# Optimization experiments

Measured on AMD Instinct MI355X. Metric: run time of the kernel, lower is better.

Reference implementation:

```python
import jax, jax.numpy as jnp
import numpy as np

N, D, H, B, TOPK, M, NLAB = 200000, 512, 512, 256, 2, 100, 2000

def setup_inputs():
    rng = np.random.default_rng(0)
    features = rng.standard_normal((N, D)).astype(np.float32) * 0.05
    labels = rng.integers(0, NLAB, size=N).astype(np.int32)
    # fixed-shape cluster membership table (replaces dynamic features[labels==lab]
    # + randperm subsampling to max_cluster_num=100 in the torch loop)
    order = np.argsort(labels, kind='stable').astype(np.int32)
    counts = np.bincount(labels, minlength=NLAB)
    offs = np.concatenate([[0], np.cumsum(counts)]).astype(np.int64)
    cluster_members = np.zeros((NLAB, M), np.int32)
    cluster_mask = np.zeros((NLAB, M), np.bool_)
    for c in range(NLAB):
        k = int(min(counts[c], M))
        cluster_members[c, :k] = order[offs[c]:offs[c] + k]
        cluster_mask[c, :k] = True
    indexes = rng.integers(0, N, size=B).astype(np.int32)
    # neighbors guaranteed != indexes so neighbor labels are never the -1 placeholder
    neighbors = ((indexes[:, None] + 1 + rng.integers(0, N - 1, size=(B, TOPK))) % N).astype(np.int32)
    all_pred = rng.random((B, TOPK)).astype(np.float32)
    # GraphConv weight [2D,H] (cat(self, agg)), classifier Linear-PReLU-Linear(2)
    W1 = (rng.standard_normal((2 * D, H)) / np.sqrt(2 * D)).astype(np.float32)
    b1 = np.zeros(H, np.float32)
    W2 = (rng.standard_normal((H, H)) / np.sqrt(H)).astype(np.float32)
    b2 = np.zeros(H, np.float32)
    prelu_a = np.full(H, 0.25, np.float32)  # PReLU default init
    W3 = (rng.standard_normal((H, 2)) / np.sqrt(H)).astype(np.float32)
    b3 = np.zeros(2, np.float32)
    arrs = dict(features=features, labels=labels, indexes=indexes, neighbors=neighbors,
                all_pred=all_pred, cluster_members=cluster_members, cluster_mask=cluster_mask,
                W1=W1, b1=b1, W2=W2, b2=b2, prelu_a=prelu_a, W3=W3, b3=b3)
    return {k: jnp.asarray(v) for k, v in arrs.items()}

def _gcnl_loss(features, labels, indexes, neighbors, all_pred, cluster_members, cluster_mask,
               W1, b1, W2, b2, prelu_a, W3, b3):
    Bn = indexes.shape[0]
    sel = all_pred >= all_pred[:, :1]                    # neighbor kept if pred[:topk] >= pred[0]
    cand = labels[neighbors]                             # [B,2] candidate labels
    dup = (cand[:, 1] == cand[:, 0]) & sel[:, 0]         # torch.unique over the <=2 selected labels
    valid = jnp.stack([sel[:, 0], sel[:, 1] & ~dup], axis=1)  # [B,2]
    members = cluster_members[cand]                      # [B,2,M]
    # labels[indexes[i]] = -1 in the loop => sample never in its own cluster
    mmask = cluster_mask[cand] & (members != indexes[:, None, None])
    mfeats = features[members] * mmask[..., None].astype(features.dtype)  # [B,2,M,D] zero-padded
    x0 = features[indexes]                               # [B,D]
    x0k = jnp.broadcast_to(x0[:, None, None, :], (Bn, TOPK, 1, x0.shape[-1]))
    x = jnp.concatenate([x0k, mfeats], axis=2)           # [B,2,M+1,D] = cat(self, cluster)
    # adj = x @ x.T ; only row 0 feeds the loss (pred[0]), zero-padded rows contribute 0
    a0 = jnp.einsum('bkd,bkmd->bkm', x[:, :, 0], x)      # [B,2,M+1] adjacency row 0
    agg0 = jnp.einsum('bkm,bkmd->bkd', a0, x)            # MeanAggregator (A @ x) row 0
    cat0 = jnp.concatenate([x[:, :, 0], agg0], axis=-1)  # [B,2,2D]
    h0 = jax.nn.relu(jnp.einsum('bkd,df->bkf', cat0, W1) + b1)  # GraphConv row 0
    z = jnp.einsum('bkf,fg->bkg', h0, W2) + b2
    z = jnp.where(z >= 0, z, prelu_a * z)                # PReLU
    logits = jnp.einsum('bkg,gc->bkc', z, W3) + b3       # [B,2,2]
    gt = (cand == -1).astype(jnp.int32)                  # labels[idx] was -1 during the loop
    logp = jax.nn.log_softmax(logits, axis=-1)
    ce = -jnp.take_along_axis(logp, gt[..., None], axis=-1)[..., 0]  # [B,2]
    loss = jnp.sum(ce * valid.astype(ce.dtype)) / Bn
    return loss * 10.0

def reference(features, labels, indexes, neighbors, all_pred, cluster_members, cluster_mask,
              W1, b1, W2, b2, prelu_a, W3, b3):
    return _gcnl_loss(features, labels, indexes, neighbors, all_pred, cluster_members, cluster_mask,
                      W1, b1, W2, b2, prelu_a, W3, b3)
```

## Files before the change

### kernel.cpp

```cpp
#include <hip/hip_runtime.h>
#include <math.h>

#define N_PTS 200000
#define D 512
#define H 512
#define BATCH 256
#define TOPK 2
#define MCAP 100

typedef __attribute__((ext_vector_type(8))) short bf16x8;
typedef __attribute__((ext_vector_type(4))) float f32x4;

__device__ inline unsigned short f2bf(float f) {
    unsigned int u = __float_as_uint(f);
    u += 0x7FFFu + ((u >> 16) & 1u);
    return (unsigned short)(u >> 16);
}

__global__ __launch_bounds__(512, 4) void gather_prep_kernel(
    const float* __restrict__ features, const int* __restrict__ labels,
    const int* __restrict__ indexes, const int* __restrict__ neighbors,
    const float* __restrict__ all_pred, const int* __restrict__ cluster_members,
    const float* __restrict__ W1, const float* __restrict__ W2,
    unsigned short* __restrict__ W1t, unsigned short* __restrict__ W2t,
    unsigned short* __restrict__ cat0, float* __restrict__ validf, int* __restrict__ gts,
    float* __restrict__ out)
{
    int bid = blockIdx.x;
    int tid = threadIdx.x;

    if (bid >= 512) {
        __shared__ float tt[2][32][33];
        int t = (bid - 512) * 2 + (tid >> 8);
        int t256 = tid & 255;
        int tx = t256 & 31, ty = t256 >> 5;
        const float* src; unsigned short* dst; int R, C, bi;
        if (t < 512) { src = W1; dst = W1t; R = 1024; C = 512; bi = t; }
        else         { src = W2; dst = W2t; R = 512;  C = 512; bi = t - 512; }
        int nbc = C >> 5;
        int br = (bi / nbc) * 32, bc = (bi % nbc) * 32;
        int half = tid >> 8;
        #pragma unroll
        for (int i = 0; i < 32; i += 8)
            tt[half][ty + i][tx] = src[(size_t)(br + ty + i) * C + bc + tx];
        __syncthreads();
        #pragma unroll
        for (int i = 0; i < 32; i += 8)
            dst[(size_t)(bc + ty + i) * R + br + tx] = f2bf(tt[half][tx][ty + i]);
        return;
    }

    int bk = bid;
    int b = bk >> 1, k = bk & 1;
    int lane = tid & 63, w = tid >> 6;

    if (bk == 0 && tid == 0) out[0] = 0.0f;

    int idx  = indexes[b];
    int nb   = neighbors[b * TOPK + k];
    int c    = labels[nb];
    int lab0 = labels[0];

    const float4* frow0 = (const float4*)(features + (size_t)idx * D);
    float4 x0a = frow0[lane * 2];
    float4 x0b = frow0[lane * 2 + 1];

    const int NITER = 13;
    int   rowv[NITER];
    float wv[NITER];
    #pragma unroll
    for (int i = 0; i < NITER; ++i) {
        int m = w + i * 8;
        int row = idx; float wt = 0.0f;
        if (m == 0) {
            wt = 1.0f;
        } else if (m <= MCAP) {
            int mm = m - 1;
            int r2 = cluster_members[c * MCAP + mm];
            bool pad  = (r2 == 0) && !(c == lab0 && mm == 0);
            bool self = (r2 == idx);
            if (!pad && !self) { row = r2; wt = 1.0f; }
        }
        rowv[i] = row; wv[i] = wt;
    }

    float agg[8] = {0,0,0,0,0,0,0,0};

    const float4* fr0 = (const float4*)(features + (size_t)rowv[0] * D);
    float4 fa = fr0[lane * 2];
    float4 fb = fr0[lane * 2 + 1];
    #pragma unroll
    for (int i = 0; i < NITER; ++i) {
        float4 ca = fa, cb = fb;
        if (i + 1 < NITER) {
            const float4* nx = (const float4*)(features + (size_t)rowv[i + 1] * D);
            fa = nx[lane * 2];
            fb = nx[lane * 2 + 1];
        }
        float p = ca.x*x0a.x + ca.y*x0a.y + ca.z*x0a.z + ca.w*x0a.w
                + cb.x*x0b.x + cb.y*x0b.y + cb.z*x0b.z + cb.w*x0b.w;
        #pragma unroll
        for (int off = 32; off >= 1; off >>= 1) p += __shfl_xor(p, off);
        p *= wv[i];
        agg[0] += p * ca.x; agg[1] += p * ca.y; agg[2] += p * ca.z; agg[3] += p * ca.w;
        agg[4] += p * cb.x; agg[5] += p * cb.y; agg[6] += p * cb.z; agg[7] += p * cb.w;
    }

    __shared__ float aggl[8][D];
    #pragma unroll
    for (int j = 0; j < 8; ++j) aggl[w][lane * 8 + j] = agg[j];
    __syncthreads();

    unsigned short* crow = cat0 + (size_t)bk * (2 * D);
    if (w == 0) {
        union { unsigned short u[8]; uint4 q; } pk;
        pk.u[0] = f2bf(x0a.x); pk.u[1] = f2bf(x0a.y); pk.u[2] = f2bf(x0a.z); pk.u[3] = f2bf(x0a.w);
        pk.u[4] = f2bf(x0b.x); pk.u[5] = f2bf(x0b.y); pk.u[6] = f2bf(x0b.z); pk.u[7] = f2bf(x0b.w);
        ((uint4*)crow)[lane] = pk.q;
    }
    {
        float v = aggl[0][tid] + aggl[1][tid] + aggl[2][tid] + aggl[3][tid]
                + aggl[4][tid] + aggl[5][tid] + aggl[6][tid] + aggl[7][tid];
        crow[D + tid] = f2bf(v);
    }
    if (tid == 0) {
        float p0 = all_pred[b * TOPK];
        float pk = all_pred[b * TOPK + k];
        int cand0 = labels[neighbors[b * TOPK]];
        bool valid;
        if (k == 0) valid = true;
        else        valid = (pk >= p0) && (c != cand0);
        validf[bk] = valid ? 1.0f : 0.0f;
        gts[bk] = (c == -1) ? 1 : 0;
    }
}

__global__ __launch_bounds__(512) void gemm1_kernel(
    const unsigned short* __restrict__ A, const unsigned short* __restrict__ Bt,
    const float* __restrict__ bias, unsigned short* __restrict__ Cb)
{
    const int N = 512, K = 1024;
    int tid = threadIdx.x;
    int lane = tid & 63, w = tid >> 6;
    int row0 = (blockIdx.x >> 4) * 32, col0 = (blockIdx.x & 15) * 32;

    int r = lane & 15;
    int kg = (lane >> 4) * 8;
    int kb = w * (K >> 3);

    const unsigned short* Ar0 = A  + (size_t)(row0 + r) * K + kb + kg;
    const unsigned short* Ar1 = Ar0 + (size_t)16 * K;
    const unsigned short* Br0 = Bt + (size_t)(col0 + r) * K + kb + kg;
    const unsigned short* Br1 = Br0 + (size_t)16 * K;

    f32x4 acc00 = {0,0,0,0}, acc01 = {0,0,0,0}, acc10 = {0,0,0,0}, acc11 = {0,0,0,0};

    #pragma unroll
    for (int ks = 0; ks < (K >> 3); ks += 32) {
        bf16x8 a0 = *(const bf16x8*)(Ar0 + ks);
        bf16x8 a1 = *(const bf16x8*)(Ar1 + ks);
        bf16x8 b0 = *(const bf16x8*)(Br0 + ks);
        bf16x8 b1 = *(const bf16x8*)(Br1 + ks);
        acc00 = __builtin_amdgcn_mfma_f32_16x16x32_bf16(a0, b0, acc00, 0, 0, 0);
        acc01 = __builtin_amdgcn_mfma_f32_16x16x32_bf16(a0, b1, acc01, 0, 0, 0);
        acc10 = __builtin_amdgcn_mfma_f32_16x16x32_bf16(a1, b0, acc10, 0, 0, 0);
        acc11 = __builtin_amdgcn_mfma_f32_16x16x32_bf16(a1, b1, acc11, 0, 0, 0);
    }

    __shared__ float red[8][32][33];
    int rbase = (lane >> 4) * 4, cbase = lane & 15;
    #pragma unroll
    for (int j = 0; j < 4; ++j) {
        red[w][rbase + j][cbase]           = acc00[j];
        red[w][rbase + j][16 + cbase]      = acc01[j];
        red[w][16 + rbase + j][cbase]      = acc10[j];
        red[w][16 + rbase + j][16 + cbase] = acc11[j];
    }
    __syncthreads();

    #pragma unroll
    for (int e = tid; e < 1024; e += 512) {
        int rr = e >> 5, cc = e & 31;
        float v = red[0][rr][cc] + red[1][rr][cc] + red[2][rr][cc] + red[3][rr][cc]
                + red[4][rr][cc] + red[5][rr][cc] + red[6][rr][cc] + red[7][rr][cc];
        int gc = col0 + cc;
        v = fmaxf(v + bias[gc], 0.0f);
        Cb[(size_t)(row0 + rr) * N + gc] = f2bf(v);
    }
}

__global__ __launch_bounds__(512) void gemm2_final_kernel(
    const unsigned short* __restrict__ A, const unsigned short* __restrict__ Bt,
    const float* __restrict__ b2, const float* __restrict__ pa,
    const float* __restrict__ W3, const float* __restrict__ b3,
    const float* __restrict__ validf, const int* __restrict__ gts,
    float* __restrict__ out)
{
    const int K = 512;
    int tid = threadIdx.x;
    int lane = tid & 63, w = tid >> 6;
    int row0 = blockIdx.x * 16;

    int r = lane & 15;
    int kg = (lane >> 4) * 8;

    const unsigned short* Ar  = A + (size_t)(row0 + r) * K + kg;
    const unsigned short* Br0 = Bt + (size_t)(w * 64 + 0  + r) * K + kg;
    const unsigned short* Br1 = Bt + (size_t)(w * 64 + 16 + r) * K + kg;
    const unsigned short* Br2 = Bt + (size_t)(w * 64 + 32 + r) * K + kg;
    const unsigned short* Br3 = Bt + (size_t)(w * 64 + 48 + r) * K + kg;

    f32x4 acc0 = {0,0,0,0}, acc1 = {0,0,0,0}, acc2 = {0,0,0,0}, acc3 = {0,0,0,0};

    #pragma unroll
    for (int ks = 0; ks < K; ks += 32) {
        bf16x8 a  = *(const bf16x8*)(Ar + ks);
        bf16x8 b0 = *(const bf16x8*)(Br0 + ks);
        bf16x8 b1 = *(const bf16x8*)(Br1 + ks);
        bf16x8 b2v = *(const bf16x8*)(Br2 + ks);
        bf16x8 b3v = *(const bf16x8*)(Br3 + ks);
        acc0 = __builtin_amdgcn_mfma_f32_16x16x32_bf16(a, b0,  acc0, 0, 0, 0);
        acc1 = __builtin_amdgcn_mfma_f32_16x16x32_bf16(a, b1,  acc1, 0, 0, 0);
        acc2 = __builtin_amdgcn_mfma_f32_16x16x32_bf16(a, b2v, acc2, 0, 0, 0);
        acc3 = __builtin_amdgcn_mfma_f32_16x16x32_bf16(a, b3v, acc3, 0, 0, 0);
    }

    float q0[4] = {0,0,0,0}, q1[4] = {0,0,0,0};
    {
        f32x4 av[4] = {acc0, acc1, acc2, acc3};
        #pragma unroll
        for (int t = 0; t < 4; ++t) {
            int gc = w * 64 + t * 16 + r;
            float bb = b2[gc], aa = pa[gc];
            float w30 = W3[gc * 2], w31 = W3[gc * 2 + 1];
            #pragma unroll
            for (int j = 0; j < 4; ++j) {
                float v = av[t][j] + bb;
                v = (v >= 0.0f) ? v : aa * v;
                q0[j] += v * w30;
                q1[j] += v * w31;
            }
        }
    }
    #pragma unroll
    for (int off = 8; off >= 1; off >>= 1) {
        #pragma unroll
        for (int j = 0; j < 4; ++j) {
            q0[j] += __shfl_xor(q0[j], off);
            q1[j] += __shfl_xor(q1[j], off);
        }
    }

    __shared__ float part[8][16][2];
    if (r == 0) {
        int rg = (lane >> 4) * 4;
        #pragma unroll
        for (int j = 0; j < 4; ++j) {
            part[w][rg + j][0] = q0[j];
            part[w][rg + j][1] = q1[j];
        }
    }
    __syncthreads();

    if (tid < 16) {
        int bk = row0 + tid;
        float l0 = b3[0], l1 = b3[1];
        #pragma unroll
        for (int q = 0; q < 8; ++q) { l0 += part[q][tid][0]; l1 += part[q][tid][1]; }
        float mx = fmaxf(l0, l1);
        float lse = mx + logf(expf(l0 - mx) + expf(l1 - mx));
        float sel = gts[bk] ? l1 : l0;
        float ce = (lse - sel) * validf[bk];
        #pragma unroll
        for (int off = 8; off >= 1; off >>= 1) ce += __shfl_xor(ce, off);
        if (tid == 0) atomicAdd(out, ce * (10.0f / (float)BATCH));
    }
}

extern "C" void kernel_launch(void* const* d_in, const int* in_sizes, int n_in,
                              void* d_out, int out_size, void* d_ws, size_t ws_size,
                              hipStream_t stream) {
    const float* features        = (const float*)d_in[0];
    const int*   labels          = (const int*)d_in[1];
    const int*   indexes         = (const int*)d_in[2];
    const int*   neighbors       = (const int*)d_in[3];
    const float* all_pred        = (const float*)d_in[4];
    const int*   cluster_members = (const int*)d_in[5];
    const float* W1 = (const float*)d_in[7];
    const float* b1 = (const float*)d_in[8];
    const float* W2 = (const float*)d_in[9];
    const float* b2 = (const float*)d_in[10];
    const float* pa = (const float*)d_in[11];
    const float* W3 = (const float*)d_in[12];
    const float* b3 = (const float*)d_in[13];
    float* out = (float*)d_out;

    char* ws = (char*)d_ws;
    float*          validf = (float*)(ws + 8192);
    int*            gts    = (int*)(ws + 10240);
    unsigned short* W1t    = (unsigned short*)(ws + 12288);
    unsigned short* W2t    = (unsigned short*)(ws + 1060864);
    unsigned short* cat0b  = (unsigned short*)(ws + 1585152);
    unsigned short* h0b    = (unsigned short*)(ws + 2633728);

    gather_prep_kernel<<<896, 512, 0, stream>>>(
        features, labels, indexes, neighbors, all_pred, cluster_members,
        W1, W2, W1t, W2t, cat0b, validf, gts, out);
    gemm1_kernel<<<256, 512, 0, stream>>>(cat0b, W1t, b1, h0b);
    gemm2_final_kernel<<<32, 512, 0, stream>>>(h0b, W2t, b2, pa, W3, b3,
                                               validf, gts, out);
}
```

Before: 49.71 us.

## Fuse first MLP GEMM into final GEMM kernel via shared-memory hidden tile

Removes the separate gemm1 launch and computes the GraphConv GEMM, ReLU, second GEMM, PReLU, classifier and loss in one 32-block kernel. Hidden activations stay in shared memory as fp32 and are converted to bf16 when loaded as MFMA operands, avoiding a global write/read of h0. In exchange, the first GEMM runs on only 32 blocks, with each block streaming the full W1 and looping over K=1024, which sharply reduces parallelism for that stage.

```diff
diff --git a/kernel.cpp b/kernel.cpp
--- a/kernel.cpp
+++ b/kernel.cpp
@@ -135,145 +135,133 @@
     }
 }
 
-__global__ __launch_bounds__(512) void gemm1_kernel(
-    const unsigned short* __restrict__ A, const unsigned short* __restrict__ Bt,
-    const float* __restrict__ bias, unsigned short* __restrict__ Cb)
-{
-    const int N = 512, K = 1024;
-    int tid = threadIdx.x;
-    int lane = tid & 63, w = tid >> 6;
-    int row0 = (blockIdx.x >> 4) * 32, col0 = (blockIdx.x & 15) * 32;
-
-    int r = lane & 15;
-    int kg = (lane >> 4) * 8;
-    int kb = w * (K >> 3);
-
-    const unsigned short* Ar0 = A  + (size_t)(row0 + r) * K + kb + kg;
-    const unsigned short* Ar1 = Ar0 + (size_t)16 * K;
-    const unsigned short* Br0 = Bt + (size_t)(col0 + r) * K + kb + kg;
-    const unsigned short* Br1 = Br0 + (size_t)16 * K;
-
-    f32x4 acc00 = {0,0,0,0}, acc01 = {0,0,0,0}, acc10 = {0,0,0,0}, acc11 = {0,0,0,0};
-
-    #pragma unroll
-    for (int ks = 0; ks < (K >> 3); ks += 32) {
-        bf16x8 a0 = *(const bf16x8*)(Ar0 + ks);
-        bf16x8 a1 = *(const bf16x8*)(Ar1 + ks);
-        bf16x8 b0 = *(const bf16x8*)(Br0 + ks);
-        bf16x8 b1 = *(const bf16x8*)(Br1 + ks);
-        acc00 = __builtin_amdgcn_mfma_f32_16x16x32_bf16(a0, b0, acc00, 0, 0, 0);
-        acc01 = __builtin_amdgcn_mfma_f32_16x16x32_bf16(a0, b1, acc01, 0, 0, 0);
-        acc10 = __builtin_amdgcn_mfma_f32_16x16x32_bf16(a1, b0, acc10, 0, 0, 0);
-        acc11 = __builtin_amdgcn_mfma_f32_16x16x32_bf16(a1, b1, acc11, 0, 0, 0);
-    }
-
-    __shared__ float red[8][32][33];
-    int rbase = (lane >> 4) * 4, cbase = lane & 15;
-    #pragma unroll
-    for (int j = 0; j < 4; ++j) {
-        red[w][rbase + j][cbase]           = acc00[j];
-        red[w][rbase + j][16 + cbase]      = acc01[j];
-        red[w][16 + rbase + j][cbase]      = acc10[j];
-        red[w][16 + rbase + j][16 + cbase] = acc11[j];
-    }
-    __syncthreads();
-
-    #pragma unroll
-    for (int e = tid; e < 1024; e += 512) {
-        int rr = e >> 5, cc = e & 31;
-        float v = red[0][rr][cc] + red[1][rr][cc] + red[2][rr][cc] + red[3][rr][cc]
-                + red[4][rr][cc] + red[5][rr][cc] + red[6][rr][cc] + red[7][rr][cc];
-        int gc = col0 + cc;
-        v = fmaxf(v + bias[gc], 0.0f);
-        Cb[(size_t)(row0 + rr) * N + gc] = f2bf(v);
-    }
-}
-
-__global__ __launch_bounds__(512) void gemm2_final_kernel(
-    const unsigned short* __restrict__ A, const unsigned short* __restrict__ Bt,
+__global__ __launch_bounds__(512) void mlp_final_kernel(
+    const unsigned short* __restrict__ A,
+    const unsigned short* __restrict__ W1t,
+    const float* __restrict__ b1,
+    const unsigned short* __restrict__ W2t,
     const float* __restrict__ b2, const float* __restrict__ pa,
     const float* __restrict__ W3, const float* __restrict__ b3,
     const float* __restrict__ validf, const int* __restrict__ gts,
     float* __restrict__ out)
 {
-    const int K = 512;
     int tid = threadIdx.x;
     int lane = tid & 63, w = tid >> 6;
     int row0 = blockIdx.x * 16;
-
     int r = lane & 15;
     int kg = (lane >> 4) * 8;
 
-    const unsigned short* Ar  = A + (size_t)(row0 + r) * K + kg;
-    const unsigned short* Br0 = Bt + (size_t)(w * 64 + 0  + r) * K + kg;
-    const unsigned short* Br1 = Bt + (size_t)(w * 64 + 16 + r) * K + kg;
-    const unsigned short* Br2 = Bt + (size_t)(w * 64 + 32 + r) * K + kg;
-    const unsigned short* Br3 = Bt + (size_t)(w * 64 + 48 + r) * K + kg;
-
-    f32x4 acc0 = {0,0,0,0}, acc1 = {0,0,0,0}, acc2 = {0,0,0,0}, acc3 = {0,0,0,0};
-
-    #pragma unroll
-    for (int ks = 0; ks < K; ks += 32) {
-        bf16x8 a  = *(const bf16x8*)(Ar + ks);
-        bf16x8 b0 = *(const bf16x8*)(Br0 + ks);
-        bf16x8 b1 = *(const bf16x8*)(Br1 + ks);
-        bf16x8 b2v = *(const bf16x8*)(Br2 + ks);
-        bf16x8 b3v = *(const bf16x8*)(Br3 + ks);
-        acc0 = __builtin_amdgcn_mfma_f32_16x16x32_bf16(a, b0,  acc0, 0, 0, 0);
-        acc1 = __builtin_amdgcn_mfma_f32_16x16x32_bf16(a, b1,  acc1, 0, 0, 0);
-        acc2 = __builtin_amdgcn_mfma_f32_16x16x32_bf16(a, b2v, acc2, 0, 0, 0);
-        acc3 = __builtin_amdgcn_mfma_f32_16x16x32_bf16(a, b3v, acc3, 0, 0, 0);
-    }
-
-    float q0[4] = {0,0,0,0}, q1[4] = {0,0,0,0};
+    __shared__ float h0s[16][514];
+    __shared__ float part[8][16][2];
+
     {
+        const int K = 1024;
+        const unsigned short* Ar  = A   + (size_t)(row0 + r) * K + kg;
+        const unsigned short* Br0 = W1t + (size_t)(w * 64 + 0  + r) * K + kg;
+        const unsigned short* Br1 = W1t + (size_t)(w * 64 + 16 + r) * K + kg;
+        const unsigned short* Br2 = W1t + (size_t)(w * 64 + 32 + r) * K + kg;
+        const unsigned short* Br3 = W1t + (size_t)(w * 64 + 48 + r) * K + kg;
+
+        f32x4 acc0 = {0,0,0,0}, acc1 = {0,0,0,0}, acc2 = {0,0,0,0}, acc3 = {0,0,0,0};
+        #pragma unroll
+        for (int ks = 0; ks < K; ks += 32) {
+            bf16x8 a   = *(const bf16x8*)(Ar + ks);
+            bf16x8 b0  = *(const bf16x8*)(Br0 + ks);
+            bf16x8 b1v = *(const bf16x8*)(Br1 + ks);
+            bf16x8 b2v = *(const bf16x8*)(Br2 + ks);
+            bf16x8 b3v = *(const bf16x8*)(Br3 + ks);
+            acc0 = __builtin_amdgcn_mfma_f32_16x16x32_bf16(a, b0,  acc0, 0, 0, 0);
+            acc1 = __builtin_amdgcn_mfma_f32_16x16x32_bf16(a, b1v, acc1, 0, 0, 0);
+            acc2 = __builtin_amdgcn_mfma_f32_16x16x32_bf16(a, b2v, acc2, 0, 0, 0);
+            acc3 = __builtin_amdgcn_mfma_f32_16x16x32_bf16(a, b3v, acc3, 0, 0, 0);
+        }
         f32x4 av[4] = {acc0, acc1, acc2, acc3};
         #pragma unroll
         for (int t = 0; t < 4; ++t) {
             int gc = w * 64 + t * 16 + r;
-            float bb = b2[gc], aa = pa[gc];
-            float w30 = W3[gc * 2], w31 = W3[gc * 2 + 1];
+            float bb = b1[gc];
             #pragma unroll
             for (int j = 0; j < 4; ++j) {
-                float v = av[t][j] + bb;
-                v = (v >= 0.0f) ? v : aa * v;
-                q0[j] += v * w30;
-                q1[j] += v * w31;
-            }
-        }
-    }
-    #pragma unroll
-    for (int off = 8; off >= 1; off >>= 1) {
-        #pragma unroll
-        for (int j = 0; j < 4; ++j) {
-            q0[j] += __shfl_xor(q0[j], off);
-            q1[j] += __shfl_xor(q1[j], off);
-        }
-    }
-
-    __shared__ float part[8][16][2];
-    if (r == 0) {
-        int rg = (lane >> 4) * 4;
-        #pragma unroll
-        for (int j = 0; j < 4; ++j) {
-            part[w][rg + j][0] = q0[j];
-            part[w][rg + j][1] = q1[j];
+                int rr = (lane >> 4) * 4 + j;
+                h0s[rr][gc] = fmaxf(av[t][j] + bb, 0.0f);
+            }
         }
     }
     __syncthreads();
 
-    if (tid < 16) {
-        int bk = row0 + tid;
-        float l0 = b3[0], l1 = b3[1];
-        #pragma unroll
-        for (int q = 0; q < 8; ++q) { l0 += part[q][tid][0]; l1 += part[q][tid][1]; }
-        float mx = fmaxf(l0, l1);
-        float lse = mx + logf(expf(l0 - mx) + expf(l1 - mx));
-        float sel = gts[bk] ? l1 : l0;
-        float ce = (lse - sel) * validf[bk];
-        #pragma unroll
-        for (int off = 8; off >= 1; off >>= 1) ce += __shfl_xor(ce, off);
-        if (tid == 0) atomicAdd(out, ce * (10.0f / (float)BATCH));
+    {
+        const int K = 512;
+        const unsigned short* Br0 = W2t + (size_t)(w * 64 + 0  + r) * K + kg;
+        const unsigned short* Br1 = W2t + (size_t)(w * 64 + 16 + r) * K + kg;
+        const unsigned short* Br2 = W2t + (size_t)(w * 64 + 32 + r) * K + kg;
+        const unsigned short* Br3 = W2t + (size_t)(w * 64 + 48 + r) * K + kg;
+
+        f32x4 acc0 = {0,0,0,0}, acc1 = {0,0,0,0}, acc2 = {0,0,0,0}, acc3 = {0,0,0,0};
+        #pragma unroll
+        for (int ks = 0; ks < K; ks += 32) {
+            bf16x8 a;
+            #pragma unroll
+            for (int j = 0; j < 8; ++j)
+                ((unsigned short*)&a)[j] = f2bf(h0s[r][ks + kg + j]);
+            bf16x8 b0  = *(const bf16x8*)(Br0 + ks);
+            bf16x8 b1v = *(const bf16x8*)(Br1 + ks);
+            bf16x8 b2v = *(const bf16x8*)(Br2 + ks);
+            bf16x8 b3v = *(const bf16x8*)(Br3 + ks);
+            acc0 = __builtin_amdgcn_mfma_f32_16x16x32_bf16(a, b0,  acc0, 0, 0, 0);
+            acc1 = __builtin_amdgcn_mfma_f32_16x16x32_bf16(a, b1v, acc1, 0, 0, 0);
+            acc2 = __builtin_amdgcn_mfma_f32_16x16x32_bf16(a, b2v, acc2, 0, 0, 0);
+            acc3 = __builtin_amdgcn_mfma_f32_16x16x32_bf16(a, b3v, acc3, 0, 0, 0);
+        }
+
+        float q0[4] = {0,0,0,0}, q1[4] = {0,0,0,0};
+        {
+            f32x4 av[4] = {acc0, acc1, acc2, acc3};
+            #pragma unroll
+            for (int t = 0; t < 4; ++t) {
+                int gc = w * 64 + t * 16 + r;
+                float bb = b2[gc], aa = pa[gc];
+                float w30 = W3[gc * 2], w31 = W3[gc * 2 + 1];
+                #pragma unroll
+                for (int j = 0; j < 4; ++j) {
+                    float v = av[t][j] + bb;
+                    v = (v >= 0.0f) ? v : aa * v;
+                    q0[j] += v * w30;
+                    q1[j] += v * w31;
+                }
+            }
+        }
+        #pragma unroll
+        for (int off = 8; off >= 1; off >>= 1) {
+            #pragma unroll
+            for (int j = 0; j < 4; ++j) {
+                q0[j] += __shfl_xor(q0[j], off);
+                q1[j] += __shfl_xor(q1[j], off);
+            }
+        }
+
+        if (r == 0) {
+            int rg = (lane >> 4) * 4;
+            #pragma unroll
+            for (int j = 0; j < 4; ++j) {
+                part[w][rg + j][0] = q0[j];
+                part[w][rg + j][1] = q1[j];
+            }
+        }
+        __syncthreads();
+
+        if (tid < 16) {
+            int bk = row0 + tid;
+            float l0 = b3[0], l1 = b3[1];
+            #pragma unroll
+            for (int q = 0; q < 8; ++q) { l0 += part[q][tid][0]; l1 += part[q][tid][1]; }
+            float mx = fmaxf(l0, l1);
+            float lse = mx + logf(expf(l0 - mx) + expf(l1 - mx));
+            float sel = gts[bk] ? l1 : l0;
+            float ce = (lse - sel) * validf[bk];
+            #pragma unroll
+            for (int off = 8; off >= 1; off >>= 1) ce += __shfl_xor(ce, off);
+            if (tid == 0) atomicAdd(out, ce * (10.0f / (float)BATCH));
+        }
     }
 }
 
@@ -301,12 +289,10 @@
     unsigned short* W1t    = (unsigned short*)(ws + 12288);
     unsigned short* W2t    = (unsigned short*)(ws + 1060864);
     unsigned short* cat0b  = (unsigned short*)(ws + 1585152);
-    unsigned short* h0b    = (unsigned short*)(ws + 2633728);
 
     gather_prep_kernel<<<896, 512, 0, stream>>>(
         features, labels, indexes, neighbors, all_pred, cluster_members,
         W1, W2, W1t, W2t, cat0b, validf, gts, out);
-    gemm1_kernel<<<256, 512, 0, stream>>>(cat0b, W1t, b1, h0b);
-    gemm2_final_kernel<<<32, 512, 0, stream>>>(h0b, W2t, b2, pa, W3, b3,
-                                               validf, gts, out);
-}
+    mlp_final_kernel<<<32, 512, 0, stream>>>(cat0b, W1t, b1, W2t, b2, pa, W3, b3,
+                                             validf, gts, out);
+}
```

After: 76.70 us. 54.3% more time.
